# Kernel optimization log

Hardware: AMD Instinct MI355X
Metric: run time of the kernel (lower is better)

## Reference

```python
import jax, jax.numpy as jnp
import numpy as np

NUM_LODS = 16
MIN_RES, MAX_RES = 16, 512
CODEBOOK = 1 << 12  # codebook_bitwidth=12
GROWTH = (MAX_RES / MIN_RES) ** (1.0 / (NUM_LODS - 1))
RES = [int(np.floor(MIN_RES * GROWTH ** l)) for l in range(NUM_LODS)]
PRIME_Y = np.uint32(2654435761)  # instant-ngp style spatial hash prime
N_POINTS = 4194304


def setup_inputs() -> dict:
    key = jax.random.key(0)
    ks = jax.random.split(key, 6)
    x = jax.random.uniform(ks[0], (N_POINTS, 2), dtype=jnp.float32)  # coords in [0,1]^2
    latents = 0.1 * jax.random.normal(ks[1], (NUM_LODS, CODEBOOK, 1), dtype=jnp.float32)
    dec_w = 0.1 * jax.random.normal(ks[2], (1, 1), dtype=jnp.float32)  # latent->feature decoder ('sq')
    dec_b = jnp.zeros((1,), dtype=jnp.float32)                          # use_shift=True
    w1 = jax.random.normal(ks[3], (16, 16), dtype=jnp.float32) / 4.0    # hidden_dim=16
    b1 = jnp.zeros((16,), dtype=jnp.float32)
    w2 = jax.random.normal(ks[4], (16, 3), dtype=jnp.float32) / 4.0     # RGB head
    b2 = jnp.zeros((3,), dtype=jnp.float32)
    return {"x": x, "latents": latents, "dec_w": dec_w, "dec_b": dec_b,
            "w1": w1, "b1": b1, "w2": w2, "b2": b2}


def _corner_index(ix, iy, res):
    # dense storage when the grid fits in the codebook, hashed otherwise
    if res * res <= CODEBOOK:
        return ix * res + iy
    h = ix.astype(jnp.uint32) ^ (iy.astype(jnp.uint32) * PRIME_Y)
    return (h % np.uint32(CODEBOOK)).astype(jnp.int32)


def _interp_lod(coords, table, res):
    # coords [N,2] in [0,1]; table [CODEBOOK, F] decoded features for this LOD
    pos = coords * (res - 1)
    p0 = jnp.floor(pos)
    frac = pos - p0
    i0 = p0.astype(jnp.int32)
    i1 = jnp.minimum(i0 + 1, res - 1)
    fx, fy = frac[:, 0:1], frac[:, 1:2]
    f00 = table[_corner_index(i0[:, 0], i0[:, 1], res)]
    f01 = table[_corner_index(i0[:, 0], i1[:, 1], res)]
    f10 = table[_corner_index(i1[:, 0], i0[:, 1], res)]
    f11 = table[_corner_index(i1[:, 0], i1[:, 1], res)]
    return (f00 * (1 - fx) * (1 - fy) + f01 * (1 - fx) * fy
            + f10 * fx * (1 - fy) + f11 * fx * fy)


def reference(x, latents, dec_w, dec_b, w1, b1, w2, b2):
    # Codebook latent decode: decode the (tiny) latent tables once, then gather.
    feat_tables = jnp.einsum('lcd,df->lcf', latents, dec_w) + dec_b  # [L, C, 1]
    feats = [_interp_lod(x, feat_tables[l], RES[l]) for l in range(NUM_LODS)]
    h = jnp.concatenate(feats, axis=-1)  # [N, 16]  (multiscale_type='cat')
    h = jax.nn.relu(h @ w1 + b1)
    return h @ w2 + b2                    # [N, 3] RGB
```

## Files before the change

### kernel.cpp

```cpp
#include <hip/hip_runtime.h>
#include <hip/hip_fp16.h>
#include <math.h>

#define CODEBOOK 4096
#define TPB 1024
#define NWAVES (TPB / 64)
#define CHUNKS 16
#define PTS_PER_BLOCK (TPB * CHUNKS)
#define N_QUAD 4
#define N_PAIR 3
#define N_DENSE 7
#define N_HASH 9
#define QMAX 2305
#define PMAX 8196
#define PRIME_B2   0x1362u

#define HL_OFF 0
#define DQ_OFF 73728
#define DP_OFF 92168
#define BN_OFF 124960
#define SMEM_BYTES 157728

#define PIN2(a,b)           asm volatile("" : "+v"(a), "+v"(b))
#define PIN8(a,b,c,d,e,f,g,i) \
    asm volatile("" : "+v"(a), "+v"(b), "+v"(c), "+v"(d), "+v"(e), "+v"(f), "+v"(g), "+v"(i))

#if defined(__has_builtin)
#if __has_builtin(__builtin_amdgcn_mfma_f32_16x16x16f16)
#define HAVE_MFMA16 1
#endif
#if __has_builtin(__builtin_elementwise_fma)
#define HAS_EFMA 1
#endif
#endif
#ifndef HAVE_MFMA16
#define HAVE_MFMA16 0
#endif

typedef _Float16 half4v  __attribute__((ext_vector_type(4)));
typedef float    float4v __attribute__((ext_vector_type(4)));
typedef float    f32x2   __attribute__((ext_vector_type(2)));

struct Params {
    int      res[16];
    float    rm1[16];
    int      q_off[N_QUAD];
    unsigned magic[N_QUAD];
    int      shift[N_QUAD];
    int      p_off[N_PAIR];
};

__device__ __forceinline__ unsigned pack2(float a, float b) {
    return (unsigned)__half_as_ushort(__float2half(a))
         | ((unsigned)__half_as_ushort(__float2half(b)) << 16);
}
__device__ __forceinline__ float cvt_lo(unsigned u) {
    return __half2float(__ushort_as_half((unsigned short)(u & 0xffffu)));
}
__device__ __forceinline__ float cvt_hi(unsigned u) {
    return __half2float(__ushort_as_half((unsigned short)(u >> 16)));
}
__device__ __forceinline__ float bilerp(float A0, float A1, float B0, float B1,
                                        float w, float v) {
    f32x2 A = {A0, A1}, B = {B0, B1}, W = {w, w};
#if defined(HAS_EFMA)
    f32x2 R = __builtin_elementwise_fma(W, B - A, A);
#else
    f32x2 R = {fmaf(w, B0 - A0, A0), fmaf(w, B1 - A1, A1)};
#endif
    return fmaf(v, R.y - R.x, R.x);
}

__global__ __launch_bounds__(TPB, 4) void shacira_fwd(
    const float* __restrict__ x,
    const float* __restrict__ latents,
    const float* __restrict__ dec_w,
    const float* __restrict__ dec_b,
    const float* __restrict__ w1,
    const float* __restrict__ b1,
    const float* __restrict__ w2,
    const float* __restrict__ b2,
    float* __restrict__ out,
    Params pr)
{
    __shared__ __align__(16) unsigned char smem[SMEM_BYTES];
    unsigned short* hl = (unsigned short*)(smem + HL_OFF);
    uint2*          dq = (uint2*)(smem + DQ_OFF);
    unsigned*       dp = (unsigned*)(smem + DP_OFF);
#if HAVE_MFMA16
    unsigned*   bounce = (unsigned*)(smem + BN_OFF);
#endif

    const int tid = threadIdx.x;
    const float dw = dec_w[0];
    const float db = dec_b[0];

    #pragma unroll
    for (int l = 0; l < N_QUAD; ++l) {
        const int res = pr.res[l];
        const int n = res * res;
        const unsigned M = pr.magic[l];
        const int sh = pr.shift[l];
        const int off = pr.q_off[l];
        const float* lat = latents + l * CODEBOOK;
        for (int e = tid; e < n; e += TPB) {
            int ix = (int)(((unsigned)e * M) >> sh);
            int iy = e - ix * res;
            int ixp = min(ix + 1, res - 1);
            int iyp = min(iy + 1, res - 1);
            const float* r0 = lat + ix * res;
            const float* r1 = lat + ixp * res;
            uint2 qv;
            qv.x = pack2(fmaf(r0[iy],  dw, db), fmaf(r1[iy],  dw, db));
            qv.y = pack2(fmaf(r0[iyp], dw, db), fmaf(r1[iyp], dw, db));
            dq[off + e] = qv;
        }
    }
    #pragma unroll
    for (int l = 0; l < N_PAIR; ++l) {
        const int res = pr.res[4 + l];
        const int n = res * res;
        const int off = pr.p_off[l];
        const float* lat = latents + (4 + l) * CODEBOOK;
        for (int e = tid; e < n; e += TPB) {
            float a = fmaf(lat[e],     dw, db);
            float b = fmaf(lat[e + 1], dw, db);
            dp[off + e] = pack2(a, b);
        }
    }
    #pragma unroll
    for (int l = 0; l < N_HASH; ++l) {
        const float* lat = latents + (N_DENSE + l) * CODEBOOK;
        for (int e = tid; e < CODEBOOK; e += TPB)
            hl[l * CODEBOOK + e] = __half_as_ushort(__float2half(fmaf(lat[e], dw, db)));
    }
    __syncthreads();

    const int lane = tid & 63;
    const int wid  = tid >> 6;
    const int q    = lane >> 4;
    const int r15  = lane & 15;
    const char* hp  = (const char*)smem;
    const char* hp8 = (const char*)smem + 65536;

#if HAVE_MFMA16
    half4v a1f, a2f;
    float4v c1f, c2f;
    #pragma unroll
    for (int j = 0; j < 4; ++j) {
        const int k = q * 4 + j;
        a1f[j] = (_Float16)w1[k * 16 + r15];
        a2f[j] = (r15 < 3) ? (_Float16)w2[k * 3 + r15] : (_Float16)0.f;
        c1f[j] = b1[k];
        c2f[j] = b2[min(k, 2)];
    }
    const int sW = (lane >> 2) & 1;
    const int sR = (r15 >> 2) & 1;
    unsigned* wbase = &bounce[wid * 512 + lane * 8];
#endif

    const int pbase0 = blockIdx.x * PTS_PER_BLOCK;
    const float2* xp = reinterpret_cast<const float2*>(x) + pbase0;
    float* outp = out + (size_t)pbase0 * 3;

    float2 xy = xp[tid];

    for (int c = 0; c < CHUNKS; ++c) {
        const int t64 = c * TPB + (tid & ~63);

        float fxs[8], fys[8];
        uint2 qvv[N_QUAD];
        unsigned pu0[N_PAIR], pu1[N_PAIR];
        unsigned h7[4];
        #pragma unroll
        for (int l = 0; l < 8; ++l) {
            const int res = pr.res[l];
            f32x2 pxy = (f32x2){xy.x, xy.y} * (f32x2){pr.rm1[l], pr.rm1[l]};
            int i0x = (int)pxy.x, i0y = (int)pxy.y;
            fxs[l] = __builtin_amdgcn_fractf(pxy.x);
            fys[l] = __builtin_amdgcn_fractf(pxy.y);
            if (l < N_QUAD) {
                qvv[l] = dq[pr.q_off[l] + (int)__umul24((unsigned)i0x, (unsigned)res) + i0y];
            } else if (l < N_DENSE) {
                int e = pr.p_off[l - 4] + (int)__umul24((unsigned)i0x, (unsigned)res) + i0y;
                pu0[l - 4] = dp[e];
                pu1[l - 4] = dp[e + res];
            } else {
                unsigned ux0b = (unsigned)(i0x << 1), ux1b = ux0b + 2u;
                unsigned hyb0 = __umul24((unsigned)i0y, PRIME_B2);
                unsigned hyb1 = hyb0 + PRIME_B2;
                h7[0] = (unsigned)*(const unsigned short*)(hp + ((ux0b ^ hyb0) & 0x1FFEu));
                h7[1] = (unsigned)*(const unsigned short*)(hp + ((ux1b ^ hyb0) & 0x1FFEu));
                h7[2] = (unsigned)*(const unsigned short*)(hp + ((ux0b ^ hyb1) & 0x1FFEu));
                h7[3] = (unsigned)*(const unsigned short*)(hp + ((ux1b ^ hyb1) & 0x1FFEu));
            }
        }
        unsigned hv[8][4];
        #pragma unroll
        for (int i = 0; i < 8; ++i) {
            const int l = 8 + i;
            f32x2 pxy = (f32x2){xy.x, xy.y} * (f32x2){pr.rm1[l], pr.rm1[l]};
            int i0x = (int)pxy.x, i0y = (int)pxy.y;
            unsigned ux0b = (unsigned)(i0x << 1), ux1b = ux0b + 2u;
            unsigned hyb0 = __umul24((unsigned)i0y, PRIME_B2);
            unsigned hyb1 = hyb0 + PRIME_B2;
            if (i < 7) {
                const char* tb = hp + 8192 * (i + 1);
                hv[i][0] = (unsigned)*(const unsigned short*)(tb + ((ux0b ^ hyb0) & 0x1FFEu));
                hv[i][1] = (unsigned)*(const unsigned short*)(tb + ((ux1b ^ hyb0) & 0x1FFEu));
                hv[i][2] = (unsigned)*(const unsigned short*)(tb + ((ux0b ^ hyb1) & 0x1FFEu));
                hv[i][3] = (unsigned)*(const unsigned short*)(tb + ((ux1b ^ hyb1) & 0x1FFEu));
            } else {
                hv[i][0] = (unsigned)*(const unsigned short*)(hp8 + ((ux0b ^ hyb0) & 0x1FFEu));
                hv[i][1] = (unsigned)*(const unsigned short*)(hp8 + ((ux1b ^ hyb0) & 0x1FFEu));
                hv[i][2] = (unsigned)*(const unsigned short*)(hp8 + ((ux0b ^ hyb1) & 0x1FFEu));
                hv[i][3] = (unsigned)*(const unsigned short*)(hp8 + ((ux1b ^ hyb1) & 0x1FFEu));
            }
        }

        const int cn = (c + 1 < CHUNKS) ? (c + 1) : c;
        float2 xy_next = xp[cn * TPB + tid];

        float h[16];

        PIN8(qvv[0].x, qvv[0].y, qvv[1].x, qvv[1].y, qvv[2].x, qvv[2].y, qvv[3].x, qvv[3].y);
        #pragma unroll
        for (int l = 0; l < N_QUAD; ++l) {
            h[l] = bilerp(cvt_lo(qvv[l].x), cvt_lo(qvv[l].y),
                          cvt_hi(qvv[l].x), cvt_hi(qvv[l].y), fxs[l], fys[l]);
        }

        PIN8(pu0[0], pu0[1], pu0[2], pu1[0], pu1[1], pu1[2], h7[0], h7[1]);
        PIN2(h7[2], h7[3]);
        #pragma unroll
        for (int l = N_QUAD; l < N_DENSE; ++l) {
            h[l] = bilerp(cvt_lo(pu0[l - 4]), cvt_lo(pu1[l - 4]),
                          cvt_hi(pu0[l - 4]), cvt_hi(pu1[l - 4]), fys[l], fxs[l]);
        }
        h[7] = bilerp(cvt_lo(h7[0]), cvt_lo(h7[1]), cvt_lo(h7[2]), cvt_lo(h7[3]),
                      fys[7], fxs[7]);

        PIN8(hv[0][0], hv[0][1], hv[0][2], hv[0][3], hv[1][0], hv[1][1], hv[1][2], hv[1][3]);
        PIN8(hv[2][0], hv[2][1], hv[2][2], hv[2][3], hv[3][0], hv[3][1], hv[3][2], hv[3][3]);
        #pragma unroll
        for (int i = 0; i < 4; ++i) {
            const int l = 8 + i;
            f32x2 pxy = (f32x2){xy.x, xy.y} * (f32x2){pr.rm1[l], pr.rm1[l]};
            float fx = __builtin_amdgcn_fractf(pxy.x);
            float fy = __builtin_amdgcn_fractf(pxy.y);
            h[l] = bilerp(cvt_lo(hv[i][0]), cvt_lo(hv[i][1]),
                          cvt_lo(hv[i][2]), cvt_lo(hv[i][3]), fy, fx);
        }

        PIN8(hv[4][0], hv[4][1], hv[4][2], hv[4][3], hv[5][0], hv[5][1], hv[5][2], hv[5][3]);
        PIN8(hv[6][0], hv[6][1], hv[6][2], hv[6][3], hv[7][0], hv[7][1], hv[7][2], hv[7][3]);
        #pragma unroll
        for (int i = 4; i < 8; ++i) {
            const int l = 8 + i;
            f32x2 pxy = (f32x2){xy.x, xy.y} * (f32x2){pr.rm1[l], pr.rm1[l]};
            float fx = __builtin_amdgcn_fractf(pxy.x);
            float fy = __builtin_amdgcn_fractf(pxy.y);
            h[l] = bilerp(cvt_lo(hv[i][0]), cvt_lo(hv[i][1]),
                          cvt_lo(hv[i][2]), cvt_lo(hv[i][3]), fy, fx);
        }

#if HAVE_MFMA16
        unsigned hw[8];
        #pragma unroll
        for (int i = 0; i < 8; ++i)
            hw[i] = __builtin_bit_cast(unsigned,
                        __builtin_amdgcn_cvt_pkrtz(h[2 * i], h[2 * i + 1]));
        *reinterpret_cast<uint4*>(wbase + sW * 4)       = uint4{hw[0], hw[1], hw[2], hw[3]};
        *reinterpret_cast<uint4*>(wbase + (sW ^ 1) * 4) = uint4{hw[4], hw[5], hw[6], hw[7]};

        #pragma unroll
        for (int t = 0; t < 4; ++t) {
            const int row = 16 * t + r15;
            const unsigned* rb = &bounce[wid * 512 + row * 8 + ((q * 2) ^ (sR * 4))];
            half4v bf = *reinterpret_cast<const half4v*>(rb);
            float4v d1 = __builtin_amdgcn_mfma_f32_16x16x16f16(a1f, bf, c1f, 0, 0, 0);
            unsigned u0 = __builtin_bit_cast(unsigned,
                              __builtin_amdgcn_cvt_pkrtz(fmaxf(d1[0], 0.f), fmaxf(d1[1], 0.f)));
            unsigned u1 = __builtin_bit_cast(unsigned,
                              __builtin_amdgcn_cvt_pkrtz(fmaxf(d1[2], 0.f), fmaxf(d1[3], 0.f)));
            uint2 uu; uu.x = u0; uu.y = u1;
            half4v rp = __builtin_bit_cast(half4v, uu);
            float4v d2 = __builtin_amdgcn_mfma_f32_16x16x16f16(a2f, rp, c2f, 0, 0, 0);
            if (lane < 16) {
                float* op = outp + (size_t)(t64 + 16 * t + r15) * 3;
                op[0] = d2[0]; op[1] = d2[1]; op[2] = d2[2];
            }
        }
#else
        float o0 = b2[0], o1 = b2[1], o2 = b2[2];
        #pragma unroll
        for (int k = 0; k < 16; ++k) {
            float acc = b1[k];
            #pragma unroll
            for (int l = 0; l < 16; ++l)
                acc = fmaf(h[l], w1[l * 16 + k], acc);
            acc = fmaxf(acc, 0.f);
            o0 = fmaf(acc, w2[k * 3 + 0], o0);
            o1 = fmaf(acc, w2[k * 3 + 1], o1);
            o2 = fmaf(acc, w2[k * 3 + 2], o2);
        }
        float* op = outp + (size_t)(t64 + lane) * 3;
        op[0] = o0; op[1] = o1; op[2] = o2;
#endif
        xy = xy_next;
    }
}

extern "C" void kernel_launch(void* const* d_in, const int* in_sizes, int n_in,
                              void* d_out, int out_size, void* d_ws, size_t ws_size,
                              hipStream_t stream)
{
    Params pr;
    const double growth = pow(512.0 / 16.0, 1.0 / 15.0);
    for (int l = 0; l < 16; ++l) {
        pr.res[l] = (int)floor(16.0 * pow(growth, (double)l));
        pr.rm1[l] = (float)(pr.res[l] - 1);
    }
    int qoff = 0;
    for (int l = 0; l < N_QUAD; ++l) {
        pr.q_off[l] = qoff;
        qoff += pr.res[l] * pr.res[l];
        const int d = pr.res[l];
        pr.magic[l] = 0; pr.shift[l] = 0;
        for (int s = 12; s <= 23; ++s) {
            unsigned long long M = ((1ull << s) + d - 1) / d;
            if ((unsigned long long)(d * d - 1) * M >= (1ull << 32)) continue;
            bool ok = true;
            for (int e = 0; e < d * d; ++e)
                if ((int)(((unsigned long long)e * M) >> s) != e / d) { ok = false; break; }
            if (ok) { pr.magic[l] = (unsigned)M; pr.shift[l] = s; break; }
        }
    }
    int poff = 0;
    for (int l = 0; l < N_PAIR; ++l) {
        pr.p_off[l] = poff;
        poff += pr.res[4 + l] * pr.res[4 + l];
    }

    const int n = in_sizes[0] / 2;
    const int blocks = n / PTS_PER_BLOCK;

    shacira_fwd<<<blocks, TPB, 0, stream>>>(
        (const float*)d_in[0], (const float*)d_in[1], (const float*)d_in[2],
        (const float*)d_in[3], (const float*)d_in[4], (const float*)d_in[5],
        (const float*)d_in[6], (const float*)d_in[7], (float*)d_out, pr);
}
```

Before: 72.33 us.

## Precompute dense quad tables in a pre-kernel and gather from global memory

```diff
diff --git a/kernel.cpp b/kernel.cpp
--- a/kernel.cpp
+++ b/kernel.cpp
@@ -7,21 +7,15 @@
 #define NWAVES (TPB / 64)
 #define CHUNKS 16
 #define PTS_PER_BLOCK (TPB * CHUNKS)
-#define N_QUAD 4
-#define N_PAIR 3
 #define N_DENSE 7
 #define N_HASH 9
-#define QMAX 2305
-#define PMAX 8196
 #define PRIME_B2   0x1362u
 
-#define HL_OFF 0
-#define DQ_OFF 73728
-#define DP_OFF 92168
-#define BN_OFF 124960
-#define SMEM_BYTES 157728
+#define BN_OFF 73728
+#define SMEM_BYTES (73728 + 32768)
 
 #define PIN2(a,b)           asm volatile("" : "+v"(a), "+v"(b))
+#define PIN4(a,b,c,d)       asm volatile("" : "+v"(a), "+v"(b), "+v"(c), "+v"(d))
 #define PIN8(a,b,c,d,e,f,g,i) \
     asm volatile("" : "+v"(a), "+v"(b), "+v"(c), "+v"(d), "+v"(e), "+v"(f), "+v"(g), "+v"(i))
 
@@ -44,10 +38,8 @@
 struct Params {
     int      res[16];
     float    rm1[16];
-    int      q_off[N_QUAD];
-    unsigned magic[N_QUAD];
-    int      shift[N_QUAD];
-    int      p_off[N_PAIR];
+    int      q_off[N_DENSE];
+    int      q_total;
 };
 
 __device__ __forceinline__ unsigned pack2(float a, float b) {
@@ -69,6 +61,32 @@
     f32x2 R = {fmaf(w, B0 - A0, A0), fmaf(w, B1 - A1, A1)};
 #endif
     return fmaf(v, R.y - R.x, R.x);
+}
+
+__global__ void stage_quads(const float* __restrict__ latents,
+                            const float* __restrict__ dec_w,
+                            const float* __restrict__ dec_b,
+                            uint2* __restrict__ gq, Params pr)
+{
+    const int t = blockIdx.x * blockDim.x + threadIdx.x;
+    if (t >= pr.q_total) return;
+    int l = 0;
+    #pragma unroll
+    for (int k = 1; k < N_DENSE; ++k) if (t >= pr.q_off[k]) l = k;
+    const int e = t - pr.q_off[l];
+    const int res = pr.res[l];
+    const float dw = dec_w[0], db = dec_b[0];
+    const int ix = e / res;
+    const int iy = e - ix * res;
+    const int ixp = min(ix + 1, res - 1);
+    const int iyp = min(iy + 1, res - 1);
+    const float* lat = latents + l * CODEBOOK;
+    const float* r0 = lat + ix * res;
+    const float* r1 = lat + ixp * res;
+    uint2 qv;
+    qv.x = pack2(fmaf(r0[iy],  dw, db), fmaf(r1[iy],  dw, db));
+    qv.y = pack2(fmaf(r0[iyp], dw, db), fmaf(r1[iyp], dw, db));
+    gq[t] = qv;
 }
 
 __global__ __launch_bounds__(TPB, 4) void shacira_fwd(
@@ -81,12 +99,11 @@
     const float* __restrict__ w2,
     const float* __restrict__ b2,
     float* __restrict__ out,
+    const uint2* __restrict__ gq,
     Params pr)
 {
     __shared__ __align__(16) unsigned char smem[SMEM_BYTES];
-    unsigned short* hl = (unsigned short*)(smem + HL_OFF);
-    uint2*          dq = (uint2*)(smem + DQ_OFF);
-    unsigned*       dp = (unsigned*)(smem + DP_OFF);
+    unsigned short* hl = (unsigned short*)smem;
 #if HAVE_MFMA16
     unsigned*   bounce = (unsigned*)(smem + BN_OFF);
 #endif
@@ -95,39 +112,6 @@
     const float dw = dec_w[0];
     const float db = dec_b[0];
 
-    #pragma unroll
-    for (int l = 0; l < N_QUAD; ++l) {
-        const int res = pr.res[l];
-        const int n = res * res;
-        const unsigned M = pr.magic[l];
-        const int sh = pr.shift[l];
-        const int off = pr.q_off[l];
-        const float* lat = latents + l * CODEBOOK;
-        for (int e = tid; e < n; e += TPB) {
-            int ix = (int)(((unsigned)e * M) >> sh);
-            int iy = e - ix * res;
-            int ixp = min(ix + 1, res - 1);
-            int iyp = min(iy + 1, res - 1);
-            const float* r0 = lat + ix * res;
-            const float* r1 = lat + ixp * res;
-            uint2 qv;
-            qv.x = pack2(fmaf(r0[iy],  dw, db), fmaf(r1[iy],  dw, db));
-            qv.y = pack2(fmaf(r0[iyp], dw, db), fmaf(r1[iyp], dw, db));
-            dq[off + e] = qv;
-        }
-    }
-    #pragma unroll
-    for (int l = 0; l < N_PAIR; ++l) {
-        const int res = pr.res[4 + l];
-        const int n = res * res;
-        const int off = pr.p_off[l];
-        const float* lat = latents + (4 + l) * CODEBOOK;
-        for (int e = tid; e < n; e += TPB) {
-            float a = fmaf(lat[e],     dw, db);
-            float b = fmaf(lat[e + 1], dw, db);
-            dp[off + e] = pack2(a, b);
-        }
-    }
     #pragma unroll
     for (int l = 0; l < N_HASH; ++l) {
         const float* lat = latents + (N_DENSE + l) * CODEBOOK;
@@ -169,31 +153,30 @@
         const int t64 = c * TPB + (tid & ~63);
 
         float fxs[8], fys[8];
-        uint2 qvv[N_QUAD];
-        unsigned pu0[N_PAIR], pu1[N_PAIR];
-        unsigned h7[4];
-        #pragma unroll
-        for (int l = 0; l < 8; ++l) {
+        uint2 qvv[N_DENSE];
+        #pragma unroll
+        for (int l = 0; l < N_DENSE; ++l) {
             const int res = pr.res[l];
             f32x2 pxy = (f32x2){xy.x, xy.y} * (f32x2){pr.rm1[l], pr.rm1[l]};
             int i0x = (int)pxy.x, i0y = (int)pxy.y;
             fxs[l] = __builtin_amdgcn_fractf(pxy.x);
             fys[l] = __builtin_amdgcn_fractf(pxy.y);
-            if (l < N_QUAD) {
-                qvv[l] = dq[pr.q_off[l] + (int)__umul24((unsigned)i0x, (unsigned)res) + i0y];
-            } else if (l < N_DENSE) {
-                int e = pr.p_off[l - 4] + (int)__umul24((unsigned)i0x, (unsigned)res) + i0y;
-                pu0[l - 4] = dp[e];
-                pu1[l - 4] = dp[e + res];
-            } else {
-                unsigned ux0b = (unsigned)(i0x << 1), ux1b = ux0b + 2u;
-                unsigned hyb0 = __umul24((unsigned)i0y, PRIME_B2);
-                unsigned hyb1 = hyb0 + PRIME_B2;
-                h7[0] = (unsigned)*(const unsigned short*)(hp + ((ux0b ^ hyb0) & 0x1FFEu));
-                h7[1] = (unsigned)*(const unsigned short*)(hp + ((ux1b ^ hyb0) & 0x1FFEu));
-                h7[2] = (unsigned)*(const unsigned short*)(hp + ((ux0b ^ hyb1) & 0x1FFEu));
-                h7[3] = (unsigned)*(const unsigned short*)(hp + ((ux1b ^ hyb1) & 0x1FFEu));
-            }
+            qvv[l] = gq[pr.q_off[l] + (int)__umul24((unsigned)i0x, (unsigned)res) + i0y];
+        }
+
+        unsigned h7[4];
+        {
+            f32x2 pxy = (f32x2){xy.x, xy.y} * (f32x2){pr.rm1[7], pr.rm1[7]};
+            int i0x = (int)pxy.x, i0y = (int)pxy.y;
+            fxs[7] = __builtin_amdgcn_fractf(pxy.x);
+            fys[7] = __builtin_amdgcn_fractf(pxy.y);
+            unsigned ux0b = (unsigned)(i0x << 1), ux1b = ux0b + 2u;
+            unsigned hyb0 = __umul24((unsigned)i0y, PRIME_B2);
+            unsigned hyb1 = hyb0 + PRIME_B2;
+            h7[0] = (unsigned)*(const unsigned short*)(hp + ((ux0b ^ hyb0) & 0x1FFEu));
+            h7[1] = (unsigned)*(const unsigned short*)(hp + ((ux1b ^ hyb0) & 0x1FFEu));
+            h7[2] = (unsigned)*(const unsigned short*)(hp + ((ux0b ^ hyb1) & 0x1FFEu));
+            h7[3] = (unsigned)*(const unsigned short*)(hp + ((ux1b ^ hyb1) & 0x1FFEu));
         }
         unsigned hv[8][4];
         #pragma unroll
@@ -223,27 +206,12 @@
 
         float h[16];
 
-        PIN8(qvv[0].x, qvv[0].y, qvv[1].x, qvv[1].y, qvv[2].x, qvv[2].y, qvv[3].x, qvv[3].y);
-        #pragma unroll
-        for (int l = 0; l < N_QUAD; ++l) {
-            h[l] = bilerp(cvt_lo(qvv[l].x), cvt_lo(qvv[l].y),
-                          cvt_hi(qvv[l].x), cvt_hi(qvv[l].y), fxs[l], fys[l]);
-        }
-
-        PIN8(pu0[0], pu0[1], pu0[2], pu1[0], pu1[1], pu1[2], h7[0], h7[1]);
-        PIN2(h7[2], h7[3]);
-        #pragma unroll
-        for (int l = N_QUAD; l < N_DENSE; ++l) {
-            h[l] = bilerp(cvt_lo(pu0[l - 4]), cvt_lo(pu1[l - 4]),
-                          cvt_hi(pu0[l - 4]), cvt_hi(pu1[l - 4]), fys[l], fxs[l]);
-        }
+        PIN8(h7[0], h7[1], h7[2], h7[3], hv[0][0], hv[0][1], hv[0][2], hv[0][3]);
+        PIN8(hv[1][0], hv[1][1], hv[1][2], hv[1][3], hv[2][0], hv[2][1], hv[2][2], hv[2][3]);
         h[7] = bilerp(cvt_lo(h7[0]), cvt_lo(h7[1]), cvt_lo(h7[2]), cvt_lo(h7[3]),
                       fys[7], fxs[7]);
-
-        PIN8(hv[0][0], hv[0][1], hv[0][2], hv[0][3], hv[1][0], hv[1][1], hv[1][2], hv[1][3]);
-        PIN8(hv[2][0], hv[2][1], hv[2][2], hv[2][3], hv[3][0], hv[3][1], hv[3][2], hv[3][3]);
-        #pragma unroll
-        for (int i = 0; i < 4; ++i) {
+        #pragma unroll
+        for (int i = 0; i < 3; ++i) {
             const int l = 8 + i;
             f32x2 pxy = (f32x2){xy.x, xy.y} * (f32x2){pr.rm1[l], pr.rm1[l]};
             float fx = __builtin_amdgcn_fractf(pxy.x);
@@ -251,17 +219,34 @@
             h[l] = bilerp(cvt_lo(hv[i][0]), cvt_lo(hv[i][1]),
                           cvt_lo(hv[i][2]), cvt_lo(hv[i][3]), fy, fx);
         }
-
-        PIN8(hv[4][0], hv[4][1], hv[4][2], hv[4][3], hv[5][0], hv[5][1], hv[5][2], hv[5][3]);
-        PIN8(hv[6][0], hv[6][1], hv[6][2], hv[6][3], hv[7][0], hv[7][1], hv[7][2], hv[7][3]);
-        #pragma unroll
-        for (int i = 4; i < 8; ++i) {
+        PIN8(hv[3][0], hv[3][1], hv[3][2], hv[3][3], hv[4][0], hv[4][1], hv[4][2], hv[4][3]);
+        #pragma unroll
+        for (int i = 3; i < 5; ++i) {
             const int l = 8 + i;
             f32x2 pxy = (f32x2){xy.x, xy.y} * (f32x2){pr.rm1[l], pr.rm1[l]};
             float fx = __builtin_amdgcn_fractf(pxy.x);
             float fy = __builtin_amdgcn_fractf(pxy.y);
             h[l] = bilerp(cvt_lo(hv[i][0]), cvt_lo(hv[i][1]),
                           cvt_lo(hv[i][2]), cvt_lo(hv[i][3]), fy, fx);
+        }
+        PIN8(hv[5][0], hv[5][1], hv[5][2], hv[5][3], hv[6][0], hv[6][1], hv[6][2], hv[6][3]);
+        PIN4(hv[7][0], hv[7][1], hv[7][2], hv[7][3]);
+        #pragma unroll
+        for (int i = 5; i < 8; ++i) {
+            const int l = 8 + i;
+            f32x2 pxy = (f32x2){xy.x, xy.y} * (f32x2){pr.rm1[l], pr.rm1[l]};
+            float fx = __builtin_amdgcn_fractf(pxy.x);
+            float fy = __builtin_amdgcn_fractf(pxy.y);
+            h[l] = bilerp(cvt_lo(hv[i][0]), cvt_lo(hv[i][1]),
+                          cvt_lo(hv[i][2]), cvt_lo(hv[i][3]), fy, fx);
+        }
+
+        PIN8(qvv[0].x, qvv[0].y, qvv[1].x, qvv[1].y, qvv[2].x, qvv[2].y, qvv[3].x, qvv[3].y);
+        PIN8(qvv[4].x, qvv[4].y, qvv[5].x, qvv[5].y, qvv[6].x, qvv[6].y, h7[0], h7[1]);
+        #pragma unroll
+        for (int l = 0; l < N_DENSE; ++l) {
+            h[l] = bilerp(cvt_lo(qvv[l].x), cvt_lo(qvv[l].y),
+                          cvt_hi(qvv[l].x), cvt_hi(qvv[l].y), fxs[l], fys[l]);
         }
 
 #if HAVE_MFMA16
@@ -322,31 +307,22 @@
         pr.rm1[l] = (float)(pr.res[l] - 1);
     }
     int qoff = 0;
-    for (int l = 0; l < N_QUAD; ++l) {
+    for (int l = 0; l < N_DENSE; ++l) {
         pr.q_off[l] = qoff;
         qoff += pr.res[l] * pr.res[l];
-        const int d = pr.res[l];
-        pr.magic[l] = 0; pr.shift[l] = 0;
-        for (int s = 12; s <= 23; ++s) {
-            unsigned long long M = ((1ull << s) + d - 1) / d;
-            if ((unsigned long long)(d * d - 1) * M >= (1ull << 32)) continue;
-            bool ok = true;
-            for (int e = 0; e < d * d; ++e)
-                if ((int)(((unsigned long long)e * M) >> s) != e / d) { ok = false; break; }
-            if (ok) { pr.magic[l] = (unsigned)M; pr.shift[l] = s; break; }
-        }
-    }
-    int poff = 0;
-    for (int l = 0; l < N_PAIR; ++l) {
-        pr.p_off[l] = poff;
-        poff += pr.res[4 + l] * pr.res[4 + l];
-    }
+    }
+    pr.q_total = qoff;
 
     const int n = in_sizes[0] / 2;
     const int blocks = n / PTS_PER_BLOCK;
+
+    uint2* gq = (uint2*)d_ws;
+
+    stage_quads<<<(pr.q_total + 255) / 256, 256, 0, stream>>>(
+        (const float*)d_in[1], (const float*)d_in[2], (const float*)d_in[3], gq, pr);
 
     shacira_fwd<<<blocks, TPB, 0, stream>>>(
         (const float*)d_in[0], (const float*)d_in[1], (const float*)d_in[2],
         (const float*)d_in[3], (const float*)d_in[4], (const float*)d_in[5],
-        (const float*)d_in[6], (const float*)d_in[7], (float*)d_out, pr);
-}
+        (const float*)d_in[6], (const float*)d_in[7], (float*)d_out, gq, pr);
+}
```

After: 80.73 us. 11.6% more time.
